# Optimization experiments

Measured on AMD Instinct MI355X. Metric: run time of the kernel, lower is better.

## Reference

```python
import jax, jax.numpy as jnp
import numpy as np


def setup_inputs() -> dict:
    key = jax.random.key(0)
    kq, kk, kv = jax.random.split(key, 3)
    B, S, D = 4, 4096, 128
    return {
        "q_proj": jax.random.normal(kq, (B, S, D), dtype=jnp.float32),
        "k_proj": jax.random.normal(kk, (B, S, D), dtype=jnp.float32),
        "v_proj": jax.random.normal(kv, (B, S, D), dtype=jnp.float32),
    }


def reference(q_proj, k_proj, v_proj):
    # Block-wise online softmax in the original is mathematically exact
    # full (non-causal) scaled dot-product attention.
    d = q_proj.shape[-1]
    scale = 1.0 / jnp.sqrt(jnp.asarray(d, dtype=q_proj.dtype))
    logits = jnp.einsum('bqd,bkd->bqk', q_proj, k_proj) * scale  # [B,S,S]
    attn = jax.nn.softmax(logits, axis=-1)
    return jnp.einsum('bqk,bkd->bqd', attn, v_proj)
```

## Files before the change

kernel.cpp:

```cpp
#include <hip/hip_runtime.h>
#include <hip/hip_bf16.h>
#include <stdint.h>

#define Bn 4
#define Sn 4096
#define Dn 128
#define SCALE ((float)(0.08838834764831843 * 1.4426950408889634))

typedef __attribute__((ext_vector_type(8)))  short short8;
typedef __attribute__((ext_vector_type(4)))  short short4v;
typedef __attribute__((ext_vector_type(4)))  float f32x4;
typedef __attribute__((ext_vector_type(16))) float f32x16;
typedef __attribute__((ext_vector_type(2)))  uint32_t uint2v;

__device__ __forceinline__ uint32_t bfround(float f){
  union { float f; uint32_t u; } a; a.f = f;
  return a.u + 0x7FFFu + ((a.u >> 16) & 1u);
}
__device__ __forceinline__ uint32_t f2bf2(float lo, float hi){
  return (bfround(hi) & 0xFFFF0000u) | (bfround(lo) >> 16);
}
__device__ __forceinline__ uint32_t f2bf2_fast(float lo, float hi){
  const uint32_t a = __float_as_uint(lo) + 0x8000u;
  const uint32_t b = __float_as_uint(hi) + 0x8000u;
  return __builtin_amdgcn_perm(b, a, 0x07060302u);
}
__device__ __forceinline__ float bf2f(short s){
  union { uint32_t u; float f; } a; a.u = ((uint32_t)(unsigned short)s) << 16; return a.f;
}
__device__ __forceinline__ float fexp2(float x){
#if __has_builtin(__builtin_amdgcn_exp2f)
  return __builtin_amdgcn_exp2f(x);
#else
  return exp2f(x);
#endif
}

__device__ __forceinline__ void gload16(const void* g, void* l){
  __builtin_amdgcn_global_load_lds(
      (const __attribute__((address_space(1))) unsigned int*)g,
      (__attribute__((address_space(3))) unsigned int*)l, 16, 0, 0);
}

__global__ void prep_kernel(const float* __restrict__ k, const float* __restrict__ v,
                            short* __restrict__ kb, short* __restrict__ vt){
  const int bid = blockIdx.x;
  const int t   = threadIdx.x;
  if (bid < 2048){
    const int i = bid*256 + t;
    const f32x4 val = ((const f32x4*)k)[i];
    uint2v o;
    o[0] = f2bf2(val[0], val[1]);
    o[1] = f2bf2(val[2], val[3]);
    *(uint2v*)(kb + 4*(size_t)i) = o;
  } else {
    __shared__ float tile[64][65];
    const int vb = bid - 2048;
    const int s0 = (vb & 63) * 64;
    const int d0 = ((vb >> 6) & 1) * 64;
    const int b  = vb >> 7;
#pragma unroll
    for (int i=0;i<16;++i){
      int lin = i*256 + t;
      int r = lin >> 6, c = lin & 63;
      tile[r][c] = v[((size_t)(b*Sn + s0 + r))*Dn + d0 + c];
    }
    __syncthreads();
#pragma unroll
    for (int i=0;i<2;++i){
      int lin = i*256 + t;
      int r = lin >> 3;
      int u = lin & 7;
      union { uint32_t w[4]; short8 s; } pk;
#pragma unroll
      for (int p=0;p<4;++p){
        int x0 = u*8 + 2*p, x1 = x0 + 1;
        int k0 = (x0 & ~15) | ((x0 & 3) | (((x0>>2)&1)<<3) | (((x0>>3)&1)<<2));
        int k1 = (x1 & ~15) | ((x1 & 3) | (((x1>>2)&1)<<3) | (((x1>>3)&1)<<2));
        pk.w[p] = f2bf2(tile[k0][r], tile[k1][r]);
      }
      *(short8*)(vt + ((size_t)(b*Dn + d0 + r))*Sn + s0 + u*8) = pk.s;
    }
  }
}

__global__ __launch_bounds__(256, 3) void fa_kernel(
    const float* __restrict__ Qg, const short* __restrict__ Kb,
    const short* __restrict__ VTb, short* __restrict__ parts,
    float* __restrict__ lparts){
  __shared__ __align__(16) char lds[32768];
  const int tid = threadIdx.x;
  const int w = tid >> 6, lane = tid & 63;
  const int ln = lane & 31, h5 = lane >> 5;
  const int idx = blockIdx.x;
  const int b   = idx & 3;
  const int u2  = idx >> 2;
  const int qt  = u2 & 31;
  const int ks  = u2 >> 5;
  const int q0  = qt * 128;
  const int start_it = ks*21 + (ks < 2 ? ks : 2);
  const int n_it     = 21 + (ks < 2 ? 1 : 0);

  short8 Qf[8];
  {
    const float* qp = Qg + ((size_t)(b*Sn + q0 + w*32 + ln))*Dn;
#pragma unroll
    for (int t=0;t<8;++t){
      const int d0 = t*16 + h5*8;
      const f32x4 a = *(const f32x4*)(qp + d0);
      const f32x4 c = *(const f32x4*)(qp + d0 + 4);
      union { uint32_t u[4]; short8 s; } pk;
      pk.u[0] = f2bf2(a[0]*SCALE, a[1]*SCALE);
      pk.u[1] = f2bf2(a[2]*SCALE, a[3]*SCALE);
      pk.u[2] = f2bf2(c[0]*SCALE, c[1]*SCALE);
      pk.u[3] = f2bf2(c[2]*SCALE, c[3]*SCALE);
      Qf[t] = pk.s;
    }
  }

  f32x16 Ot[4];
#pragma unroll
  for (int m=0;m<4;++m)
#pragma unroll
    for (int r=0;r<16;++r) Ot[m][r] = 0.0f;
  float ls0=0.f, ls1=0.f, ls2=0.f, ls3=0.f;

  int goff[4], loff[4];
  const char* gbase;
  if (w < 2){
#pragma unroll
    for (int i=0;i<4;++i){
      const int ch = i*128 + w*64 + lane;
      const int r  = ch >> 4;
      const int gc = (ch & 15) ^ (r & 7);
      goff[i] = r*256 + gc*16;
      loff[i] = ch*16;
    }
    gbase = (const char*)Kb + ((size_t)(b*Sn + start_it*32))*256;
  } else {
#pragma unroll
    for (int i=0;i<4;++i){
      const int ch = i*128 + (w-2)*64 + lane;
      const int r  = ch >> 2;
      const int gc = (ch & 3) ^ ((r >> 1) & 3);
      goff[i] = r*8192 + gc*16;
      loff[i] = 8192 + ch*16;
    }
    gbase = (const char*)VTb + (size_t)b*Dn*Sn*2 + (size_t)start_it*64;
  }

  auto stage = [&](int i, int ph){
    char* ldsb = lds + ph*16384;
    const char* gb = gbase + (w < 2 ? (size_t)i*8192 : (size_t)i*64);
#pragma unroll
    for (int u=0;u<4;++u) gload16(gb + goff[u], ldsb + loff[u]);
  };

  stage(0, 0);

  for (int i=0; i<n_it; ++i){
    const int ph = i & 1;
    __syncthreads();
    if (i+1 < n_it) stage(i+1, ph^1);

    const char* bK = lds + ph*16384;
    const char* bV = bK + 8192;

    f32x16 St;
#pragma unroll
    for (int r=0;r<16;++r) St[r] = 0.0f;
#pragma unroll
    for (int t=0;t<8;++t){
      const int pos = ((2*t + h5) ^ (ln & 7)) * 16;
      const short8 kf = *(const short8*)(bK + (size_t)ln*256 + pos);
      St = __builtin_amdgcn_mfma_f32_32x32x16_bf16(kf, Qf[t], St, 0, 0, 0);
    }

#pragma unroll
    for (int r=0;r<16;++r) St[r] = fexp2(St[r]);
#pragma unroll
    for (int r=0;r<16;r+=4){
      ls0 += St[r]; ls1 += St[r+1]; ls2 += St[r+2]; ls3 += St[r+3];
    }

#pragma unroll
    for (int t=0;t<2;++t){
      union { uint32_t u[4]; short8 s; } pf;
      pf.u[0] = f2bf2_fast(St[8*t+0], St[8*t+1]);
      pf.u[1] = f2bf2_fast(St[8*t+2], St[8*t+3]);
      pf.u[2] = f2bf2_fast(St[8*t+4], St[8*t+5]);
      pf.u[3] = f2bf2_fast(St[8*t+6], St[8*t+7]);
      const int phys = ((2*t + h5) ^ ((ln >> 1) & 3)) * 16;
#pragma unroll
      for (int mt=0;mt<4;++mt){
        const short8 vf = *(const short8*)(bV + (size_t)(mt*32+ln)*64 + phys);
        Ot[mt] = __builtin_amdgcn_mfma_f32_32x32x16_bf16(vf, pf.s, Ot[mt], 0, 0, 0);
      }
    }
  }

  float lsum = (ls0 + ls1) + (ls2 + ls3);
  lsum += __shfl_xor(lsum, 32, 64);

  const int pslot = (b*32 + qt)*6 + ks;
  short* pbase = parts + (size_t)pslot*16384 + (size_t)(w*32 + ln)*128;
#pragma unroll
  for (int mt=0;mt<4;++mt){
#pragma unroll
    for (int g=0;g<4;++g){
      union { uint32_t u[2]; short4v s; } o;
      o.u[0] = f2bf2(Ot[mt][4*g],   Ot[mt][4*g+1]);
      o.u[1] = f2bf2(Ot[mt][4*g+2], Ot[mt][4*g+3]);
      *(short4v*)(pbase + mt*32 + 8*g + 4*h5) = o.s;
    }
  }
  if (h5 == 0) lparts[(size_t)pslot*128 + w*32 + ln] = lsum;
}

__global__ void reduce_kernel(const short* __restrict__ parts,
                              const float* __restrict__ lparts,
                              float* __restrict__ out){
  const int t  = threadIdx.x;
  const int s  = blockIdx.x >> 3;
  const int qg = (blockIdx.x & 7)*16 + (t >> 4);
  const int d0 = (t & 15) * 8;
  float acc[8];
#pragma unroll
  for (int j=0;j<8;++j) acc[j] = 0.0f;
  float lsum = 0.0f;
#pragma unroll
  for (int ks=0;ks<6;++ks){
    const short8 p = *(const short8*)(parts + ((size_t)(s*6+ks))*16384 + (size_t)qg*128 + d0);
#pragma unroll
    for (int j=0;j<8;++j) acc[j] += bf2f(p[j]);
    lsum += lparts[(size_t)(s*6+ks)*128 + qg];
  }
  const float linv = 1.0f / lsum;
  f32x4 o0, o1;
#pragma unroll
  for (int j=0;j<4;++j){ o0[j] = acc[j]*linv; o1[j] = acc[4+j]*linv; }
  float* op = out + ((size_t)(s*128 + qg))*128 + d0;
  *(f32x4*)op = o0;
  *(f32x4*)(op + 4) = o1;
}

extern "C" void kernel_launch(void* const* d_in, const int* in_sizes, int n_in,
                              void* d_out, int out_size, void* d_ws, size_t ws_size,
                              hipStream_t stream){
  const float* q = (const float*)d_in[0];
  const float* k = (const float*)d_in[1];
  const float* v = (const float*)d_in[2];
  float* out = (float*)d_out;
  char* ws = (char*)d_ws;
  short* kb     = (short*)ws;
  short* vt     = kb + (size_t)Bn*Sn*Dn;
  short* parts  = (short*)(ws + 8388608);
  float* lparts = (float*)(ws + 8388608 + 25165824);

  prep_kernel<<<2560, 256, 0, stream>>>(k, v, kb, vt);
  fa_kernel<<<768, 256, 0, stream>>>(q, kb, vt, parts, lparts);
  reduce_kernel<<<1024, 256, 0, stream>>>(parts, lparts, out);
}
```

Measured before the change: 121.8 us.

## Halve waves per block, give each wave two query tiles sharing K/V fragments

The attention kernel now runs 128 threads per block instead of 256. Each wave handles 64 query rows as two 32-row tiles, so every K and V fragment read from LDS feeds two MFMAs, halving LDS read traffic per FLOP. Staging is rewritten so one wave loads K and the other loads V, with 8 loads each. s_setprio is raised around the MFMA sections. The cost is roughly double the accumulator registers per wave and fewer waves to hide latency, which may reduce occupancy.

Measured after the change: 147.2 us. 1.21x slower.

```diff
diff --git a/kernel.cpp b/kernel.cpp
--- a/kernel.cpp
+++ b/kernel.cpp
@@ -84,7 +84,7 @@
   }
 }
 
-__global__ __launch_bounds__(256, 3) void fa_kernel(
+__global__ __launch_bounds__(128, 2) void fa_kernel(
     const float* __restrict__ Qg, const short* __restrict__ Kb,
     const short* __restrict__ VTb, short* __restrict__ parts,
     float* __restrict__ lparts){
@@ -101,9 +101,10 @@
   const int start_it = ks*21 + (ks < 2 ? ks : 2);
   const int n_it     = 21 + (ks < 2 ? 1 : 0);
 
-  short8 Qf[8];
-  {
-    const float* qp = Qg + ((size_t)(b*Sn + q0 + w*32 + ln))*Dn;
+  short8 Qf[2][8];
+#pragma unroll
+  for (int tile=0;tile<2;++tile){
+    const float* qp = Qg + ((size_t)(b*Sn + q0 + w*64 + tile*32 + ln))*Dn;
 #pragma unroll
     for (int t=0;t<8;++t){
       const int d0 = t*16 + h5*8;
@@ -114,46 +115,45 @@
       pk.u[1] = f2bf2(a[2]*SCALE, a[3]*SCALE);
       pk.u[2] = f2bf2(c[0]*SCALE, c[1]*SCALE);
       pk.u[3] = f2bf2(c[2]*SCALE, c[3]*SCALE);
-      Qf[t] = pk.s;
-    }
-  }
-
-  f32x16 Ot[4];
-#pragma unroll
-  for (int m=0;m<4;++m)
-#pragma unroll
-    for (int r=0;r<16;++r) Ot[m][r] = 0.0f;
-  float ls0=0.f, ls1=0.f, ls2=0.f, ls3=0.f;
-
-  int goff[4], loff[4];
+      Qf[tile][t] = pk.s;
+    }
+  }
+
+  f32x16 Ot[2][4];
+#pragma unroll
+  for (int tile=0;tile<2;++tile)
+#pragma unroll
+    for (int m=0;m<4;++m)
+#pragma unroll
+      for (int r=0;r<16;++r) Ot[tile][m][r] = 0.0f;
+  float lsA0=0.f, lsB0=0.f, lsA1=0.f, lsB1=0.f;
+
+  int goffb, loffb;
   const char* gbase;
-  if (w < 2){
-#pragma unroll
-    for (int i=0;i<4;++i){
-      const int ch = i*128 + w*64 + lane;
-      const int r  = ch >> 4;
-      const int gc = (ch & 15) ^ (r & 7);
-      goff[i] = r*256 + gc*16;
-      loff[i] = ch*16;
-    }
+  if (w == 0){
+    const int l4 = lane >> 4;
+    goffb = l4*256 + (((lane & 15) ^ l4) * 16);
+    loffb = lane*16;
     gbase = (const char*)Kb + ((size_t)(b*Sn + start_it*32))*256;
   } else {
-#pragma unroll
-    for (int i=0;i<4;++i){
-      const int ch = i*128 + (w-2)*64 + lane;
-      const int r  = ch >> 2;
-      const int gc = (ch & 3) ^ ((r >> 1) & 3);
-      goff[i] = r*8192 + gc*16;
-      loff[i] = 8192 + ch*16;
-    }
+    goffb = (lane >> 2)*8192 + ((((lane & 3) ^ ((lane >> 3) & 3))) * 16);
+    loffb = 8192 + lane*16;
     gbase = (const char*)VTb + (size_t)b*Dn*Sn*2 + (size_t)start_it*64;
   }
 
   auto stage = [&](int i, int ph){
-    char* ldsb = lds + ph*16384;
-    const char* gb = gbase + (w < 2 ? (size_t)i*8192 : (size_t)i*64);
-#pragma unroll
-    for (int u=0;u<4;++u) gload16(gb + goff[u], ldsb + loff[u]);
+    char* ldsb = lds + ph*16384 + loffb;
+    if (w == 0){
+      const char* gb = gbase + (size_t)i*8192;
+#pragma unroll
+      for (int u=0;u<8;++u)
+        gload16(gb + u*1024 + (goffb ^ ((u & 1) << 6)), ldsb + u*1024);
+    } else {
+      const char* gb = gbase + (size_t)i*64;
+#pragma unroll
+      for (int u=0;u<8;++u)
+        gload16(gb + u*131072 + goffb, ldsb + u*1024);
+    }
   };
 
   stage(0, 0);
@@ -166,55 +166,78 @@
     const char* bK = lds + ph*16384;
     const char* bV = bK + 8192;
 
-    f32x16 St;
-#pragma unroll
-    for (int r=0;r<16;++r) St[r] = 0.0f;
+    f32x16 St0, St1;
+#pragma unroll
+    for (int r=0;r<16;++r){ St0[r] = 0.0f; St1[r] = 0.0f; }
+    __builtin_amdgcn_s_setprio(1);
 #pragma unroll
     for (int t=0;t<8;++t){
       const int pos = ((2*t + h5) ^ (ln & 7)) * 16;
       const short8 kf = *(const short8*)(bK + (size_t)ln*256 + pos);
-      St = __builtin_amdgcn_mfma_f32_32x32x16_bf16(kf, Qf[t], St, 0, 0, 0);
-    }
-
-#pragma unroll
-    for (int r=0;r<16;++r) St[r] = fexp2(St[r]);
-#pragma unroll
-    for (int r=0;r<16;r+=4){
-      ls0 += St[r]; ls1 += St[r+1]; ls2 += St[r+2]; ls3 += St[r+3];
-    }
-
+      St0 = __builtin_amdgcn_mfma_f32_32x32x16_bf16(kf, Qf[0][t], St0, 0, 0, 0);
+      St1 = __builtin_amdgcn_mfma_f32_32x32x16_bf16(kf, Qf[1][t], St1, 0, 0, 0);
+    }
+    __builtin_amdgcn_s_setprio(0);
+
+#pragma unroll
+    for (int r=0;r<16;++r) St0[r] = fexp2(St0[r]);
+#pragma unroll
+    for (int r=0;r<16;++r) St1[r] = fexp2(St1[r]);
+#pragma unroll
+    for (int r=0;r<16;r+=2){
+      lsA0 += St0[r]; lsB0 += St0[r+1];
+      lsA1 += St1[r]; lsB1 += St1[r+1];
+    }
+
+    union { uint32_t u[4]; short8 s; } pf0[2], pf1[2];
 #pragma unroll
     for (int t=0;t<2;++t){
-      union { uint32_t u[4]; short8 s; } pf;
-      pf.u[0] = f2bf2_fast(St[8*t+0], St[8*t+1]);
-      pf.u[1] = f2bf2_fast(St[8*t+2], St[8*t+3]);
-      pf.u[2] = f2bf2_fast(St[8*t+4], St[8*t+5]);
-      pf.u[3] = f2bf2_fast(St[8*t+6], St[8*t+7]);
+      pf0[t].u[0] = f2bf2_fast(St0[8*t+0], St0[8*t+1]);
+      pf0[t].u[1] = f2bf2_fast(St0[8*t+2], St0[8*t+3]);
+      pf0[t].u[2] = f2bf2_fast(St0[8*t+4], St0[8*t+5]);
+      pf0[t].u[3] = f2bf2_fast(St0[8*t+6], St0[8*t+7]);
+      pf1[t].u[0] = f2bf2_fast(St1[8*t+0], St1[8*t+1]);
+      pf1[t].u[1] = f2bf2_fast(St1[8*t+2], St1[8*t+3]);
+      pf1[t].u[2] = f2bf2_fast(St1[8*t+4], St1[8*t+5]);
+      pf1[t].u[3] = f2bf2_fast(St1[8*t+6], St1[8*t+7]);
+    }
+
+    __builtin_amdgcn_s_setprio(1);
+#pragma unroll
+    for (int t=0;t<2;++t){
       const int phys = ((2*t + h5) ^ ((ln >> 1) & 3)) * 16;
 #pragma unroll
       for (int mt=0;mt<4;++mt){
         const short8 vf = *(const short8*)(bV + (size_t)(mt*32+ln)*64 + phys);
-        Ot[mt] = __builtin_amdgcn_mfma_f32_32x32x16_bf16(vf, pf.s, Ot[mt], 0, 0, 0);
+        Ot[0][mt] = __builtin_amdgcn_mfma_f32_32x32x16_bf16(vf, pf0[t].s, Ot[0][mt], 0, 0, 0);
+        Ot[1][mt] = __builtin_amdgcn_mfma_f32_32x32x16_bf16(vf, pf1[t].s, Ot[1][mt], 0, 0, 0);
       }
     }
-  }
-
-  float lsum = (ls0 + ls1) + (ls2 + ls3);
-  lsum += __shfl_xor(lsum, 32, 64);
+    __builtin_amdgcn_s_setprio(0);
+  }
+
+  float lsum0 = lsA0 + lsB0; lsum0 += __shfl_xor(lsum0, 32, 64);
+  float lsum1 = lsA1 + lsB1; lsum1 += __shfl_xor(lsum1, 32, 64);
 
   const int pslot = (b*32 + qt)*6 + ks;
-  short* pbase = parts + (size_t)pslot*16384 + (size_t)(w*32 + ln)*128;
-#pragma unroll
-  for (int mt=0;mt<4;++mt){
-#pragma unroll
-    for (int g=0;g<4;++g){
-      union { uint32_t u[2]; short4v s; } o;
-      o.u[0] = f2bf2(Ot[mt][4*g],   Ot[mt][4*g+1]);
-      o.u[1] = f2bf2(Ot[mt][4*g+2], Ot[mt][4*g+3]);
-      *(short4v*)(pbase + mt*32 + 8*g + 4*h5) = o.s;
-    }
-  }
-  if (h5 == 0) lparts[(size_t)pslot*128 + w*32 + ln] = lsum;
+#pragma unroll
+  for (int tile=0;tile<2;++tile){
+    short* pbase = parts + (size_t)pslot*16384 + (size_t)(w*64 + tile*32 + ln)*128;
+#pragma unroll
+    for (int mt=0;mt<4;++mt){
+#pragma unroll
+      for (int g=0;g<4;++g){
+        union { uint32_t u[2]; short4v s; } o;
+        o.u[0] = f2bf2(Ot[tile][mt][4*g],   Ot[tile][mt][4*g+1]);
+        o.u[1] = f2bf2(Ot[tile][mt][4*g+2], Ot[tile][mt][4*g+3]);
+        *(short4v*)(pbase + mt*32 + 8*g + 4*h5) = o.s;
+      }
+    }
+  }
+  if (h5 == 0){
+    lparts[(size_t)pslot*128 + w*64 + ln]      = lsum0;
+    lparts[(size_t)pslot*128 + w*64 + 32 + ln] = lsum1;
+  }
 }
 
 __global__ void reduce_kernel(const short* __restrict__ parts,
@@ -258,6 +281,6 @@
   float* lparts = (float*)(ws + 8388608 + 25165824);
 
   prep_kernel<<<2560, 256, 0, stream>>>(k, v, kb, vt);
-  fa_kernel<<<768, 256, 0, stream>>>(q, kb, vt, parts, lparts);
+  fa_kernel<<<768, 128, 0, stream>>>(q, kb, vt, parts, lparts);
   reduce_kernel<<<1024, 256, 0, stream>>>(parts, lparts, out);
 }
```

## Pre-swizzle K into MFMA fragment layout and load it directly from global

Applied to the files above, without the earlier changes.

The prep kernel now writes K in bf16 with a fragment-major layout, so each lane's MFMA operand is a contiguous 16-byte chunk. The attention kernel reads K fragments straight from global/L2 instead of staging them through LDS, which halves the LDS buffer and the per-iteration async copies. s_setprio is added around the MFMA sections. The cost is that global K loads now sit on the critical path inside the loop without double-buffered prefetch, which could expose latency.

After: 131.0 us. 7.5% more time.

```diff
diff --git a/kernel.cpp b/kernel.cpp
--- a/kernel.cpp
+++ b/kernel.cpp
@@ -46,16 +46,27 @@
                             short* __restrict__ kb, short* __restrict__ vt){
   const int bid = blockIdx.x;
   const int t   = threadIdx.x;
-  if (bid < 2048){
-    const int i = bid*256 + t;
-    const f32x4 val = ((const f32x4*)k)[i];
-    uint2v o;
-    o[0] = f2bf2(val[0], val[1]);
-    o[1] = f2bf2(val[2], val[3]);
-    *(uint2v*)(kb + 4*(size_t)i) = o;
+  if (bid < 512){
+    const int b = bid >> 7, i = bid & 127;
+#pragma unroll
+    for (int it=0; it<2; ++it){
+      const int lin = it*256 + t;
+      const int ln = lin & 31;
+      const int tg = lin >> 5;
+      const int tt = tg >> 1, hh = tg & 1;
+      const float* src = k + ((size_t)(b*Sn + i*32 + ln))*Dn + tg*8;
+      const f32x4 a = *(const f32x4*)src;
+      const f32x4 c = *(const f32x4*)(src + 4);
+      union { uint32_t u[4]; short8 s; } pk;
+      pk.u[0] = f2bf2(a[0], a[1]);
+      pk.u[1] = f2bf2(a[2], a[3]);
+      pk.u[2] = f2bf2(c[0], c[1]);
+      pk.u[3] = f2bf2(c[2], c[3]);
+      *(short8*)(kb + (((size_t)(b*128 + i)*8 + tt)*64 + (hh*32 + ln))*8) = pk.s;
+    }
   } else {
     __shared__ float tile[64][65];
-    const int vb = bid - 2048;
+    const int vb = bid - 512;
     const int s0 = (vb & 63) * 64;
     const int d0 = ((vb >> 6) & 1) * 64;
     const int b  = vb >> 7;
@@ -88,7 +99,7 @@
     const float* __restrict__ Qg, const short* __restrict__ Kb,
     const short* __restrict__ VTb, short* __restrict__ parts,
     float* __restrict__ lparts){
-  __shared__ __align__(16) char lds[32768];
+  __shared__ __align__(16) char lds[16384];
   const int tid = threadIdx.x;
   const int w = tid >> 6, lane = tid & 63;
   const int ln = lane & 31, h5 = lane >> 5;
@@ -125,35 +136,25 @@
     for (int r=0;r<16;++r) Ot[m][r] = 0.0f;
   float ls0=0.f, ls1=0.f, ls2=0.f, ls3=0.f;
 
-  int goff[4], loff[4];
-  const char* gbase;
-  if (w < 2){
-#pragma unroll
-    for (int i=0;i<4;++i){
-      const int ch = i*128 + w*64 + lane;
-      const int r  = ch >> 4;
-      const int gc = (ch & 15) ^ (r & 7);
-      goff[i] = r*256 + gc*16;
-      loff[i] = ch*16;
-    }
-    gbase = (const char*)Kb + ((size_t)(b*Sn + start_it*32))*256;
-  } else {
-#pragma unroll
-    for (int i=0;i<4;++i){
-      const int ch = i*128 + (w-2)*64 + lane;
+  int soff[2], doff[2];
+  {
+#pragma unroll
+    for (int u=0;u<2;++u){
+      const int ch = w*128 + u*64 + lane;
       const int r  = ch >> 2;
       const int gc = (ch & 3) ^ ((r >> 1) & 3);
-      goff[i] = r*8192 + gc*16;
-      loff[i] = 8192 + ch*16;
-    }
-    gbase = (const char*)VTb + (size_t)b*Dn*Sn*2 + (size_t)start_it*64;
-  }
+      soff[u] = r*8192 + gc*16;
+      doff[u] = ch*16;
+    }
+  }
+  const char* gbaseV = (const char*)VTb + (size_t)b*Dn*Sn*2 + (size_t)start_it*64;
+  const short* Kbase = Kb + (size_t)(b*128 + start_it)*4096 + (size_t)lane*8;
 
   auto stage = [&](int i, int ph){
-    char* ldsb = lds + ph*16384;
-    const char* gb = gbase + (w < 2 ? (size_t)i*8192 : (size_t)i*64);
-#pragma unroll
-    for (int u=0;u<4;++u) gload16(gb + goff[u], ldsb + loff[u]);
+    char* ldsb = lds + ph*8192;
+    const char* gb = gbaseV + (size_t)i*64;
+#pragma unroll
+    for (int u=0;u<2;++u) gload16(gb + soff[u], ldsb + doff[u]);
   };
 
   stage(0, 0);
@@ -163,18 +164,19 @@
     __syncthreads();
     if (i+1 < n_it) stage(i+1, ph^1);
 
-    const char* bK = lds + ph*16384;
-    const char* bV = bK + 8192;
+    const char* bV = lds + ph*8192;
+    const short* Kp = Kbase + (size_t)i*4096;
 
     f32x16 St;
 #pragma unroll
     for (int r=0;r<16;++r) St[r] = 0.0f;
+    __builtin_amdgcn_s_setprio(1);
 #pragma unroll
     for (int t=0;t<8;++t){
-      const int pos = ((2*t + h5) ^ (ln & 7)) * 16;
-      const short8 kf = *(const short8*)(bK + (size_t)ln*256 + pos);
+      const short8 kf = *(const short8*)(Kp + t*512);
       St = __builtin_amdgcn_mfma_f32_32x32x16_bf16(kf, Qf[t], St, 0, 0, 0);
     }
+    __builtin_amdgcn_s_setprio(0);
 
 #pragma unroll
     for (int r=0;r<16;++r) St[r] = fexp2(St[r]);
@@ -183,6 +185,7 @@
       ls0 += St[r]; ls1 += St[r+1]; ls2 += St[r+2]; ls3 += St[r+3];
     }
 
+    __builtin_amdgcn_s_setprio(1);
 #pragma unroll
     for (int t=0;t<2;++t){
       union { uint32_t u[4]; short8 s; } pf;
@@ -197,6 +200,7 @@
         Ot[mt] = __builtin_amdgcn_mfma_f32_32x32x16_bf16(vf, pf.s, Ot[mt], 0, 0, 0);
       }
     }
+    __builtin_amdgcn_s_setprio(0);
   }
 
   float lsum = (ls0 + ls1) + (ls2 + ls3);
@@ -257,7 +261,7 @@
   short* parts  = (short*)(ws + 8388608);
   float* lparts = (float*)(ws + 8388608 + 25165824);
 
-  prep_kernel<<<2560, 256, 0, stream>>>(k, v, kb, vt);
+  prep_kernel<<<1024, 256, 0, stream>>>(k, v, kb, vt);
   fa_kernel<<<768, 256, 0, stream>>>(q, kb, vt, parts, lparts);
   reduce_kernel<<<1024, 256, 0, stream>>>(parts, lparts, out);
 }
```
